# Optimization experiments

Measured on AMD Instinct MI355X. Metric: run time of the kernel, lower is better.

The kernel has to match this reference:

```python
import jax, jax.numpy as jnp
import numpy as np

NUM_HEADS = 32
NUM_KV_HEADS = 8
HEAD_DIM = 96
ROPE_BASE = 10000.0


def setup_inputs() -> dict:
    key = jax.random.key(0)
    k1, k2, k3 = jax.random.split(key, 3)
    B, S, H = 2, 2048, 3072
    op_size = NUM_HEADS * HEAD_DIM + 2 * NUM_KV_HEADS * HEAD_DIM  # 4608
    hidden_states = jax.random.normal(k1, (B, S, H), dtype=jnp.float32)
    w_qkv = jax.random.normal(k2, (op_size, H), dtype=jnp.float32) * (H ** -0.5)
    w_o = jax.random.normal(k3, (H, H), dtype=jnp.float32) * (H ** -0.5)
    position_ids = jnp.broadcast_to(jnp.arange(S, dtype=jnp.int64), (B, S))
    return {"hidden_states": hidden_states, "position_ids": position_ids,
            "w_qkv": w_qkv, "w_o": w_o}


def _rotate_half(x):
    x1, x2 = jnp.split(x, 2, axis=-1)
    return jnp.concatenate((-x2, x1), axis=-1)


def reference(hidden_states, position_ids, w_qkv, w_o):
    B, S, H = hidden_states.shape
    nh, nkv, hd = NUM_HEADS, NUM_KV_HEADS, HEAD_DIM
    n_rep = nh // nkv

    # fused QKV projection (torch Linear: x @ W^T)
    qkv = jnp.einsum('bsh,oh->bso', hidden_states, w_qkv)
    q_pos = nh * hd
    q = qkv[..., :q_pos].reshape(B, S, nh, hd).transpose(0, 2, 1, 3)
    k = qkv[..., q_pos:q_pos + nkv * hd].reshape(B, S, nkv, hd).transpose(0, 2, 1, 3)
    v = qkv[..., q_pos + nkv * hd:].reshape(B, S, nkv, hd).transpose(0, 2, 1, 3)

    # rotary embedding (Phi3RotaryEmbedding, rope_scaling=None)
    inv_freq = 1.0 / (ROPE_BASE ** (jnp.arange(0, hd, 2, dtype=jnp.float32) / hd))
    freqs = position_ids.astype(jnp.float32)[:, :, None] * inv_freq[None, None, :]  # [B,S,hd/2]
    emb = jnp.concatenate((freqs, freqs), axis=-1)  # [B,S,hd]
    cos = jnp.cos(emb)[:, None, :, :]  # unsqueeze head dim
    sin = jnp.sin(emb)[:, None, :, :]
    q = q * cos + _rotate_half(q) * sin
    k = k * cos + _rotate_half(k) * sin

    # repeat_kv: (B, nkv, S, hd) -> (B, nh, S, hd)
    k = jnp.repeat(k, n_rep, axis=1)
    v = jnp.repeat(v, n_rep, axis=1)

    # causal SDPA
    scale = 1.0 / jnp.sqrt(jnp.float32(hd))
    scores = jnp.einsum('bhqd,bhkd->bhqk', q, k) * scale
    causal = jnp.tril(jnp.ones((S, S), dtype=bool))
    scores = jnp.where(causal[None, None], scores, jnp.finfo(scores.dtype).min)
    probs = jax.nn.softmax(scores, axis=-1)
    attn = jnp.einsum('bhqk,bhkd->bhqd', probs, v)  # [B,nh,S,hd]

    attn = attn.transpose(0, 2, 1, 3).reshape(B, S, nh * hd)
    return jnp.einsum('bsh,oh->bso', attn, w_o)
```

## Files before the change

### kernel.cpp

```cpp
#include <hip/hip_runtime.h>
#include <stdint.h>
#include <math.h>

#define B_   2
#define S_   2048
#define H_   3072
#define NH   32
#define NKV  8
#define HD   96
#define OPSZ 4608
#define MM   (B_*S_)

typedef __attribute__((ext_vector_type(8))) short short8;
typedef __attribute__((ext_vector_type(4))) float floatx4;

__device__ __forceinline__ short f2bf(float f) {
    union { float f; uint32_t u; } v; v.f = f;
    uint32_t r = v.u + 0x7fffu + ((v.u >> 16) & 1u);
    return (short)(r >> 16);
}
__device__ __forceinline__ float bf2f(short s) {
    union { uint32_t u; float f; } v; v.u = ((uint32_t)(uint16_t)s) << 16;
    return v.f;
}
__device__ __forceinline__ uint32_t pk_bf_trunc(float lo, float hi) {
    union { float f; uint32_t u; } a, b; a.f = lo; b.f = hi;
    return (a.u >> 16) | (b.u & 0xFFFF0000u);
}
__device__ __forceinline__ float fast_exp2(float x) {
    float r;
    asm volatile("v_exp_f32 %0, %1" : "=v"(r) : "v"(x));
    return r;
}
__device__ __forceinline__ float dpp_max16(float x) {
    union { float f; int i; } a, t;
    a.f = x;
    t.i = __builtin_amdgcn_update_dpp(0, a.i, 0x128, 0xF, 0xF, false); a.f = fmaxf(a.f, t.f);
    t.i = __builtin_amdgcn_update_dpp(0, a.i, 0x124, 0xF, 0xF, false); a.f = fmaxf(a.f, t.f);
    t.i = __builtin_amdgcn_update_dpp(0, a.i, 0x122, 0xF, 0xF, false); a.f = fmaxf(a.f, t.f);
    t.i = __builtin_amdgcn_update_dpp(0, a.i, 0x121, 0xF, 0xF, false); a.f = fmaxf(a.f, t.f);
    return a.f;
}

__device__ __forceinline__ void async_load16(const void* g, void* l) {
    __builtin_amdgcn_global_load_lds(
        (const __attribute__((address_space(1))) void*)g,
        (__attribute__((address_space(3))) void*)l, 16, 0, 0);
}

#define CN1 (MM * H_ / 4)
#define CN2 (OPSZ * H_ / 4)
#define CN3 (H_ * H_ / 4)
__global__ void cast3_f32_bf16(const float* __restrict__ s1, const float* __restrict__ s2,
                               const float* __restrict__ s3, short* __restrict__ d1,
                               short* __restrict__ d2, short* __restrict__ d3) {
    int gid = blockIdx.x * blockDim.x + threadIdx.x;
    int stride = gridDim.x * blockDim.x;
    for (int i = gid; i < CN1; i += stride) {
        float4 v = ((const float4*)s1)[i];
        short4 o; o.x = f2bf(v.x); o.y = f2bf(v.y); o.z = f2bf(v.z); o.w = f2bf(v.w);
        ((short4*)d1)[i] = o;
    }
    for (int i = gid; i < CN2; i += stride) {
        float4 v = ((const float4*)s2)[i];
        short4 o; o.x = f2bf(v.x); o.y = f2bf(v.y); o.z = f2bf(v.z); o.w = f2bf(v.w);
        ((short4*)d2)[i] = o;
    }
    for (int i = gid; i < CN3; i += stride) {
        float4 v = ((const float4*)s3)[i];
        short4 o; o.x = f2bf(v.x); o.y = f2bf(v.y); o.z = f2bf(v.z); o.w = f2bf(v.w);
        ((short4*)d3)[i] = o;
    }
}

template<int BN, int OUT_BF16>
__global__ __launch_bounds__(512, 2) void gemmN(const short* __restrict__ A, const short* __restrict__ Bm,
                                                float* __restrict__ Cf, short* __restrict__ Cb,
                                                int M, int N, int K) {
    constexpr int NF    = BN / 32;
    constexpr int BSUB  = BN / 8;
    constexpr int BBY   = BN * 128;
    constexpr int JB    = (BSUB + 7) / 8;
    __shared__ __align__(16) char smem[65536 + 2 * BBY];
    const int tid = threadIdx.x;
    const int w = tid >> 6, l = tid & 63;
    const int L15 = l & 15, quad = l >> 4;
    const int wr = w & 3, wc = w >> 2;

    const int gm = M >> 8;
    const int nwg = gridDim.x;
    const int id = blockIdx.x;
    const int qq = nwg >> 3, rr = nwg & 7;
    const int xcd = id & 7, sidx = id >> 3;
    const int wgid = (xcd < rr ? xcd * (qq + 1) : rr * (qq + 1) + (xcd - rr) * qq) + sidx;
    const int m0 = (wgid % gm) << 8;
    const int n0 = (wgid / gm) * BN;

    const int cbl = ((l & 3) * 16) ^ (((l >> 5) & 1) << 5);
    uint32_t aofs[4], bofs[JB];
    #pragma unroll
    for (int j = 0; j < 4; j++) {
        const int s = j * 8 + w;
        const int row = ((s >> 1) << 4) + (l >> 2);
        const int colb = ((s & 1) << 6) + cbl;
        aofs[j] = (uint32_t)(m0 + row) * (uint32_t)(K * 2) + colb;
    }
    #pragma unroll
    for (int j = 0; j < JB; j++) {
        const int s = j * 8 + w;
        const int sc = (s < BSUB) ? s : 0;
        const int row = ((sc >> 1) << 4) + (l >> 2);
        const int colb = ((sc & 1) << 6) + cbl;
        bofs[j] = (uint32_t)(n0 + row) * (uint32_t)(K * 2) + colb;
    }
    char* ldsA = (char*)smem;
    char* ldsB = (char*)smem + 65536;

    const int lane_off = L15 * 64 + ((quad * 16) ^ (((L15 >> 3) & 1) << 5));
    const int aoff = (wr * 4) * 2048 + lane_off;
    const int boff = (wc * NF) * 2048 + lane_off;

    floatx4 acc[4][NF];
    #pragma unroll
    for (int i = 0; i < 4; i++)
        #pragma unroll
        for (int j = 0; j < NF; j++)
            acc[i][j] = (floatx4){0.f, 0.f, 0.f, 0.f};

    auto stageA = [&](int kt, int buf) {
        const uint32_t kb = (uint32_t)kt << 7;
        #pragma unroll
        for (int j = 0; j < 4; j++)
            async_load16((const char*)A + (size_t)(aofs[j] + kb),
                         ldsA + buf * 32768 + (j * 8 + w) * 1024);
    };
    auto stageB = [&](int kt, int buf) {
        const uint32_t kb = (uint32_t)kt << 7;
        #pragma unroll
        for (int j = 0; j < JB; j++)
            if (j * 8 + w < BSUB)
                async_load16((const char*)Bm + (size_t)(bofs[j] + kb),
                             ldsB + buf * BBY + (j * 8 + w) * 1024);
    };

    const int nkt = K >> 6;
    stageB(0, 0); stageA(0, 0);
    stageB(1, 1); stageA(1, 1);

    for (int t = 0; t < nkt; t++) {
        const int c = t & 1;
        const char* ab = ldsA + c * 32768 + aoff;
        const char* bb = ldsB + c * BBY + boff;

        if (BN == 288) asm volatile("s_waitcnt vmcnt(8)" ::: "memory");
        else           asm volatile("s_waitcnt vmcnt(7)" ::: "memory");
        __builtin_amdgcn_s_barrier();
        __builtin_amdgcn_sched_barrier(0);

        short8 a[4][2], bring[3][2];
        #pragma unroll
        for (int i = 0; i < 4; i++)
            #pragma unroll
            for (int kk = 0; kk < 2; kk++)
                a[i][kk] = *(const short8*)(ab + i * 2048 + kk * 1024);
        #pragma unroll
        for (int kk = 0; kk < 2; kk++)
            bring[0][kk] = *(const short8*)(bb + kk * 1024);

        #pragma unroll
        for (int g = 0; g < NF - 1; g++) {
            #pragma unroll
            for (int kk = 0; kk < 2; kk++)
                bring[(g + 1) % 3][kk] = *(const short8*)(bb + (g + 1) * 2048 + kk * 1024);
            __builtin_amdgcn_s_setprio(1);
            #pragma unroll
            for (int kk = 0; kk < 2; kk++)
                #pragma unroll
                for (int i = 0; i < 4; i++)
                    acc[i][g] = __builtin_amdgcn_mfma_f32_16x16x32_bf16(a[i][kk], bring[g % 3][kk], acc[i][g], 0, 0, 0);
            __builtin_amdgcn_s_setprio(0);
        }
        __builtin_amdgcn_sched_barrier(0);
        __builtin_amdgcn_s_barrier();
        __builtin_amdgcn_sched_barrier(0);
        if (t + 2 < nkt) { stageB(t + 2, c); stageA(t + 2, c); }
        __builtin_amdgcn_s_setprio(1);
        #pragma unroll
        for (int kk = 0; kk < 2; kk++)
            #pragma unroll
            for (int i = 0; i < 4; i++)
                acc[i][NF - 1] = __builtin_amdgcn_mfma_f32_16x16x32_bf16(a[i][kk], bring[(NF - 1) % 3][kk], acc[i][NF - 1], 0, 0, 0);
        __builtin_amdgcn_s_setprio(0);
    }
    asm volatile("s_waitcnt vmcnt(0)" ::: "memory");

    #pragma unroll
    for (int i = 0; i < 4; i++)
        #pragma unroll
        for (int j = 0; j < NF; j++)
            #pragma unroll
            for (int r = 0; r < 4; r++) {
                const int row = m0 + wr * 64 + i * 16 + quad * 4 + r;
                const int col = n0 + wc * (BN / 2) + j * 16 + L15;
                const float v = acc[i][j][r];
                if (OUT_BF16) Cb[(size_t)row * N + col] = f2bf(v);
                else          Cf[(size_t)row * N + col] = v;
            }
}

__global__ __launch_bounds__(256) void rope_vt(const short* __restrict__ qkv, const int* __restrict__ pos_ids,
                                               short* __restrict__ Q, short* __restrict__ Kc,
                                               short* __restrict__ Vt) {
    const int blk = blockIdx.x;
    const int tid = threadIdx.x;
    if (blk < B_ * S_) {
        __shared__ float2 ltab[48];
        const int s = blk % S_, b = blk / S_;
        if (tid < 48) {
            float inv = exp2f((float)tid * -0.2768273412f);
            float theta = (float)pos_ids[blk] * inv;
            float sn, cs;
            __sincosf(theta, &sn, &cs);
            ltab[tid] = make_float2(cs, sn);
        }
        __syncthreads();
        const short* row = qkv + (size_t)blk * OPSZ;
        #pragma unroll 2
        for (int i = tid; i < (NH + NKV) * 48; i += 256) {
            const int h_all = i / 48, fi = i % 48;
            const int off = (h_all < NH) ? (h_all * HD + fi) : (H_ + (h_all - NH) * HD + fi);
            float x1 = bf2f(row[off]);
            float x2 = bf2f(row[off + 48]);
            float2 t = ltab[fi];
            float o1 = x1 * t.x - x2 * t.y;
            float o2 = x2 * t.x + x1 * t.y;
            if (h_all < NH) {
                o1 *= 0.14724438747f;
                o2 *= 0.14724438747f;
                size_t qa = ((size_t)(b * NH + h_all) * S_ + s) * HD + fi;
                Q[qa]      = f2bf(o1);
                Q[qa + 48] = f2bf(o2);
            } else {
                const int kvh = h_all - NH;
                size_t kb_ = ((size_t)(b * NKV + kvh) * S_ + s) * 128;
                const int d2 = fi + 48;
                Kc[kb_ + (((fi >> 3) + s) & 15) * 8 + (fi & 7)] = f2bf(o1);
                Kc[kb_ + (((d2 >> 3) + s) & 15) * 8 + (d2 & 7)] = f2bf(o2);
            }
        }
    } else {
        __shared__ short tile[64 * 104];
        const int vblk = blk - B_ * S_;
        const int st  = vblk & 31;
        const int kvh = (vblk >> 5) & 7;
        const int b   = vblk >> 8;
        const int s0  = st * 64;
        #pragma unroll
        for (int i = 0; i < 3; i++) {
            int c = tid + i * 256;
            int row = c / 12, col8 = c % 12;
            *(short8*)&tile[row * 104 + col8 * 8] =
                *(const short8*)(qkv + (size_t)(b * S_ + s0 + row) * OPSZ + 3840 + kvh * HD + col8 * 8);
        }
        __syncthreads();
        #pragma unroll
        for (int i = 0; i < 3; i++) {
            int c = tid + i * 256;
            int d = c >> 3, col8 = c & 7;
            int chunk0 = (col8 - d) & 7;
            short8 v;
            #pragma unroll
            for (int j = 0; j < 8; j++) {
                int col0 = chunk0 * 8 + j;
                int n = ((col0 >> 5) << 1) | (col0 & 1);
                int t = (col0 & 31) >> 1;
                v[j] = tile[(n * 16 + t) * 104 + d];
            }
            *(short8*)(Vt + ((size_t)(b * NKV + kvh) * HD + d) * S_ + s0 + col8 * 8) = v;
        }
    }
}

__global__ __launch_bounds__(256) void flash_attn(const short* __restrict__ Q, const short* __restrict__ Kc,
                                                  const short* __restrict__ Vt, short* __restrict__ attn) {
    __shared__ short kl[2][64 * 128];
    __shared__ short vl[2][112 * 64];
    __shared__ short pl[4][32 * 72];
    const int x = blockIdx.x, h = blockIdx.y, b = blockIdx.z;
    const int kvh = h >> 2;
    const int tid = threadIdx.x, wave = tid >> 6, lane = tid & 63;
    const int L15 = lane & 15, quad = lane >> 4;

    #pragma unroll
    for (int i = 0; i < 2; i++) {
        uint32_t* p = (uint32_t*)&vl[i][96 * 64];
        #pragma unroll
        for (int k = 0; k < 2; k++) {
            int idx = tid + k * 256;
            p[idx] = (idx < 32) ? 0x3F803F80u : 0u;
        }
    }

    const short* kbase = Kc + (size_t)(b * NKV + kvh) * S_ * 128;
    const short* vbase = Vt + (size_t)(b * NKV + kvh) * HD * S_;
    const int klane   = lane * 8;
    const int vrow_lo = lane >> 3;
    const int vcol    = (lane & 7) * 8;

    int rotK[3], rotV[2];
    #pragma unroll
    for (int kk = 0; kk < 3; kk++) rotK[kk] = ((kk * 4 + quad + L15) & 15) * 8;
    #pragma unroll
    for (int kk = 0; kk < 2; kk++) rotV[kk] = ((kk * 4 + quad + L15) & 7) * 8;

    auto stage = [&](int kv0, int buf) {
        const short* ksrc = kbase + (size_t)kv0 * 128;
        #pragma unroll
        for (int i = 0; i < 4; i++) {
            int ck = wave * 4 + i;
            async_load16(ksrc + ck * 512 + klane, &kl[buf][ck * 512]);
        }
        #pragma unroll
        for (int i = 0; i < 3; i++) {
            int ck = wave * 3 + i;
            async_load16(vbase + (size_t)(ck * 8 + vrow_lo) * S_ + kv0 + vcol, &vl[buf][ck * 512]);
        }
    };

    #pragma unroll
    for (int pp = 0; pp < 2; pp++) {
        const int qt = pp ? x : (15 - x);
        const int q0 = qt * 128;
        const int jmax = 2 * qt + 2;

        short8 qf[2][3];
        #pragma unroll
        for (int mm = 0; mm < 2; mm++) {
            const short* qrow = Q + ((size_t)(b * NH + h) * S_ + q0 + wave * 32 + mm * 16 + L15) * HD;
            #pragma unroll
            for (int kk = 0; kk < 3; kk++) qf[mm][kk] = *(const short8*)(qrow + kk * 32 + quad * 8);
        }
        floatx4 o[2][7];
        float m_r[2][4];
        #pragma unroll
        for (int mm = 0; mm < 2; mm++) {
            #pragma unroll
            for (int nn = 0; nn < 7; nn++) o[mm][nn] = (floatx4){0.f, 0.f, 0.f, 0.f};
            #pragma unroll
            for (int r = 0; r < 4; r++) m_r[mm][r] = -3.0e38f;
        }

        __syncthreads();
        stage(0, 0);

        for (int j = 0; j < jmax; j++) {
            const int c = j & 1;
            const int kv0 = j * 64;
            __syncthreads();
            if (j + 1 < jmax) stage(kv0 + 64, 1 - c);

            const short* klp = kl[c];
            const short* vlp = vl[c];

            floatx4 sacc[2][4];
            #pragma unroll
            for (int mm = 0; mm < 2; mm++)
                #pragma unroll
                for (int n = 0; n < 4; n++) sacc[mm][n] = (floatx4){0.f, 0.f, 0.f, 0.f};
            #pragma unroll
            for (int n = 0; n < 4; n++)
                #pragma unroll
                for (int kk = 0; kk < 3; kk++) {
                    short8 kf = *(const short8*)&klp[(n * 16 + L15) * 128 + rotK[kk]];
                    sacc[0][n] = __builtin_amdgcn_mfma_f32_16x16x32_bf16(qf[0][kk], kf, sacc[0][n], 0, 0, 0);
                    sacc[1][n] = __builtin_amdgcn_mfma_f32_16x16x32_bf16(qf[1][kk], kf, sacc[1][n], 0, 0, 0);
                }

            #pragma unroll
            for (int mm = 0; mm < 2; mm++) {
                const int tbase = q0 + wave * 32 + mm * 16;
                if (kv0 + 63 > tbase) {
                    int qr_base = tbase + quad * 4;
                    #pragma unroll
                    for (int n = 0; n < 4; n++) {
                        int kv = kv0 + n * 16 + L15;
                        #pragma unroll
                        for (int r = 0; r < 4; r++)
                            if (kv > qr_base + r) sacc[mm][n][r] = -3.0e38f;
                    }
                }
                float alpha[4];
                #pragma unroll
                for (int r = 0; r < 4; r++) {
                    float mx = fmaxf(fmaxf(sacc[mm][0][r], sacc[mm][1][r]),
                                     fmaxf(sacc[mm][2][r], sacc[mm][3][r]));
                    mx = dpp_max16(mx);
                    float mn = fmaxf(m_r[mm][r], mx);
                    alpha[r] = fast_exp2(m_r[mm][r] - mn);
                    m_r[mm][r] = mn;
                }
                #pragma unroll
                for (int n = 0; n < 4; n++)
                    #pragma unroll
                    for (int r = 0; r < 4; r++)
                        sacc[mm][n][r] = fast_exp2(sacc[mm][n][r] - m_r[mm][r]);
                #pragma unroll
                for (int r = 0; r < 4; r++) {
                    int prow = mm * 16 + quad * 4 + r;
                    *(uint32_t*)&pl[wave][prow * 72 + 2 * L15]      = pk_bf_trunc(sacc[mm][0][r], sacc[mm][1][r]);
                    *(uint32_t*)&pl[wave][prow * 72 + 32 + 2 * L15] = pk_bf_trunc(sacc[mm][2][r], sacc[mm][3][r]);
                }
                #pragma unroll
                for (int nn = 0; nn < 7; nn++)
                    #pragma unroll
                    for (int r = 0; r < 4; r++) o[mm][nn][r] *= alpha[r];
            }

            #pragma unroll
            for (int kk = 0; kk < 2; kk++) {
                short8 af0 = *(const short8*)&pl[wave][L15 * 72 + kk * 32 + quad * 8];
                short8 af1 = *(const short8*)&pl[wave][(16 + L15) * 72 + kk * 32 + quad * 8];
                #pragma unroll
                for (int nn = 0; nn < 7; nn++) {
                    short8 vf = *(const short8*)&vlp[(nn * 16 + L15) * 64 + rotV[kk]];
                    o[0][nn] = __builtin_amdgcn_mfma_f32_16x16x32_bf16(af0, vf, o[0][nn], 0, 0, 0);
                    o[1][nn] = __builtin_amdgcn_mfma_f32_16x16x32_bf16(af1, vf, o[1][nn], 0, 0, 0);
                }
            }
        }

        #pragma unroll
        for (int mm = 0; mm < 2; mm++) {
            float inv_l[4];
            #pragma unroll
            for (int r = 0; r < 4; r++) {
                float l = __shfl(o[mm][6][r], lane & 48);
                inv_l[r] = 1.0f / l;
            }
            #pragma unroll
            for (int nn = 0; nn < 6; nn++)
                #pragma unroll
                for (int r = 0; r < 4; r++) {
                    float v = o[mm][nn][r] * inv_l[r];
                    int row = q0 + wave * 32 + mm * 16 + quad * 4 + r;
                    attn[((size_t)(b * S_) + row) * H_ + h * HD + nn * 16 + L15] = f2bf(v);
                }
        }
    }
}

extern "C" void kernel_launch(void* const* d_in, const int* in_sizes, int n_in,
                              void* d_out, int out_size, void* d_ws, size_t ws_size,
                              hipStream_t stream) {
    const float* hid  = (const float*)d_in[0];
    const int*   pos  = (const int*)d_in[1];
    const float* wqkv = (const float*)d_in[2];
    const float* wo   = (const float*)d_in[3];
    float* out = (float*)d_out;
    char* ws = (char*)d_ws;

    short* hid_b  = (short*)(ws + 0L);
    short* wqkv_b = (short*)(ws + 25165824L);
    short* wo_b   = (short*)(ws + 53477376L);
    short* qkv_b  = (short*)(ws + 72351744L);
    short* q_b    = (short*)(ws + 110100480L);
    short* k_b    = (short*)(ws + 135266304L);
    short* vt_b   = (short*)(ws + 143654912L);
    short* attn_b = (short*)(ws + 0L);

    cast3_f32_bf16<<<4096, 256, 0, stream>>>(hid, wqkv, wo, hid_b, wqkv_b, wo_b);

    gemmN<288, 1><<<256, 512, 0, stream>>>(hid_b, wqkv_b, nullptr, qkv_b, MM, OPSZ, H_);

    rope_vt<<<B_ * S_ + 512, 256, 0, stream>>>(qkv_b, pos, q_b, k_b, vt_b);

    flash_attn<<<dim3(8, NH, B_), 256, 0, stream>>>(q_b, k_b, vt_b, attn_b);

    gemmN<192, 0><<<256, 512, 0, stream>>>(attn_b, wo_b, out, nullptr, MM, H_, H_);
}
```

Measured before the change: 464.7 us.

## Restructure GEMM inner loop into three phased LDS-read/MFMA clusters with barriers

Replaces the rotating three-slot B fragment ring in the GEMM main loop with three grouped phases. Each phase loads a block of B fragments from LDS, waits on lgkmcnt, then issues a dense MFMA cluster, and workgroup barriers are inserted between phases to keep waves in lockstep. The global prefetch for tile t+2 is issued after the second batch of LDS reads. The aim is larger MFMA bursts and less interleaved LDS latency, at the cost of more barriers, more live registers for the B fragments, and an assumption that NF is divisible by 3.

```diff
diff --git a/kernel.cpp b/kernel.cpp
--- a/kernel.cpp
+++ b/kernel.cpp
@@ -78,6 +78,7 @@
                                                 float* __restrict__ Cf, short* __restrict__ Cb,
                                                 int M, int N, int K) {
     constexpr int NF    = BN / 32;
+    constexpr int G     = NF / 3;
     constexpr int BSUB  = BN / 8;
     constexpr int BBY   = BN * 128;
     constexpr int JB    = (BSUB + 7) / 8;
@@ -157,31 +158,43 @@
         __builtin_amdgcn_s_barrier();
         __builtin_amdgcn_sched_barrier(0);
 
-        short8 a[4][2], bring[3][2];
+        short8 a[4][2], b0[G][2], b1[G][2], b2[G][2];
         #pragma unroll
         for (int i = 0; i < 4; i++)
             #pragma unroll
             for (int kk = 0; kk < 2; kk++)
                 a[i][kk] = *(const short8*)(ab + i * 2048 + kk * 1024);
         #pragma unroll
+        for (int g = 0; g < G; g++)
+            #pragma unroll
+            for (int kk = 0; kk < 2; kk++)
+                b0[g][kk] = *(const short8*)(bb + g * 2048 + kk * 1024);
+        __builtin_amdgcn_s_barrier();
+        asm volatile("s_waitcnt lgkmcnt(0)" ::: "memory");
+        __builtin_amdgcn_sched_barrier(0);
+        __builtin_amdgcn_s_setprio(1);
+        #pragma unroll
         for (int kk = 0; kk < 2; kk++)
-            bring[0][kk] = *(const short8*)(bb + kk * 1024);
-
-        #pragma unroll
-        for (int g = 0; g < NF - 1; g++) {
+            #pragma unroll
+            for (int i = 0; i < 4; i++)
+                #pragma unroll
+                for (int g = 0; g < G; g++)
+                    acc[i][g] = __builtin_amdgcn_mfma_f32_16x16x32_bf16(a[i][kk], b0[g][kk], acc[i][g], 0, 0, 0);
+        __builtin_amdgcn_s_setprio(0);
+        __builtin_amdgcn_s_barrier();
+        __builtin_amdgcn_sched_barrier(0);
+        #pragma unroll
+        for (int g = 0; g < G; g++)
             #pragma unroll
             for (int kk = 0; kk < 2; kk++)
-                bring[(g + 1) % 3][kk] = *(const short8*)(bb + (g + 1) * 2048 + kk * 1024);
-            __builtin_amdgcn_s_setprio(1);
+                b1[g][kk] = *(const short8*)(bb + (G + g) * 2048 + kk * 1024);
+        #pragma unroll
+        for (int g = 0; g < G; g++)
             #pragma unroll
             for (int kk = 0; kk < 2; kk++)
-                #pragma unroll
-                for (int i = 0; i < 4; i++)
-                    acc[i][g] = __builtin_amdgcn_mfma_f32_16x16x32_bf16(a[i][kk], bring[g % 3][kk], acc[i][g], 0, 0, 0);
-            __builtin_amdgcn_s_setprio(0);
-        }
-        __builtin_amdgcn_sched_barrier(0);
+                b2[g][kk] = *(const short8*)(bb + (2 * G + g) * 2048 + kk * 1024);
         __builtin_amdgcn_s_barrier();
+        asm volatile("s_waitcnt lgkmcnt(0)" ::: "memory");
         __builtin_amdgcn_sched_barrier(0);
         if (t + 2 < nkt) { stageB(t + 2, c); stageA(t + 2, c); }
         __builtin_amdgcn_s_setprio(1);
@@ -189,7 +202,20 @@
         for (int kk = 0; kk < 2; kk++)
             #pragma unroll
             for (int i = 0; i < 4; i++)
-                acc[i][NF - 1] = __builtin_amdgcn_mfma_f32_16x16x32_bf16(a[i][kk], bring[(NF - 1) % 3][kk], acc[i][NF - 1], 0, 0, 0);
+                #pragma unroll
+                for (int g = 0; g < G; g++)
+                    acc[i][G + g] = __builtin_amdgcn_mfma_f32_16x16x32_bf16(a[i][kk], b1[g][kk], acc[i][G + g], 0, 0, 0);
+        __builtin_amdgcn_s_setprio(0);
+        __builtin_amdgcn_s_barrier();
+        __builtin_amdgcn_sched_barrier(0);
+        __builtin_amdgcn_s_setprio(1);
+        #pragma unroll
+        for (int kk = 0; kk < 2; kk++)
+            #pragma unroll
+            for (int i = 0; i < 4; i++)
+                #pragma unroll
+                for (int g = 0; g < G; g++)
+                    acc[i][2 * G + g] = __builtin_amdgcn_mfma_f32_16x16x32_bf16(a[i][kk], b2[g][kk], acc[i][2 * G + g], 0, 0, 0);
         __builtin_amdgcn_s_setprio(0);
     }
     asm volatile("s_waitcnt vmcnt(0)" ::: "memory");
```

After: 472.0 us. No clear change (+1.6%).
